# Optimization experiments

Measured on AMD Instinct MI355X. Metric: run time of the kernel, lower is better.

Reference implementation:

```python
import jax, jax.numpy as jnp
import numpy as np

H = 1024   # hidden size
E = 8      # num experts
B, S = 4, 2048


def setup_inputs() -> dict:
    key = jax.random.key(0)
    k1, k2, k3, k4 = jax.random.split(key, 4)
    x = jax.random.normal(k1, (B, S, H), dtype=jnp.float32)
    wg = jax.random.normal(k2, (H, E), dtype=jnp.float32) * 0.02      # gate weight
    W = jax.random.normal(k3, (E, H, H), dtype=jnp.float32) * 0.02    # expert Linear weights (out, in) per expert
    b = jax.random.normal(k4, (E, H), dtype=jnp.float32) * 0.02       # expert Linear biases
    return {"x": x, "wg": wg, "W": W, "b": b}


def reference(x, wg, W, b):
    Bb, Ss, Hh = x.shape
    Ee = wg.shape[1]
    T = Bb * Ss
    C = T // Ee  # capacity (capacity_factor = 1.0, top-1)

    xt = x.reshape(T, Hh)
    logits = xt @ wg                                   # [T, E]
    probs = jax.nn.softmax(logits, axis=-1)            # [T, E]
    idx = jnp.argmax(probs, axis=-1)                   # [T] top-1 expert
    mask = jax.nn.one_hot(idx, Ee, dtype=xt.dtype)     # [T, E]

    # position of each token within its expert's queue (0-based)
    locations = jnp.cumsum(mask, axis=0) - mask        # [T, E]
    # drop tokens over capacity
    mask = mask * (locations < C).astype(xt.dtype)
    gate = jnp.sum(probs * mask, axis=-1)              # [T] gate prob (0 if dropped)
    loc_s = jnp.sum(locations * mask, axis=-1).astype(jnp.int32)  # [T]
    loc_oh = jax.nn.one_hot(loc_s, C, dtype=xt.dtype)  # [T, C]

    dispatch = mask[:, :, None] * loc_oh[:, None, :]   # [T, E, C]
    combine = gate[:, None, None] * dispatch           # [T, E, C]

    # dispatch tokens -> per-expert buffers [E, C, H]
    exp_in = jnp.einsum('tec,th->ech', dispatch, xt)
    # per-expert Linear: y = x @ W_e^T + b_e
    exp_out = jnp.einsum('ech,efh->ecf', exp_in, W) + b[:, None, :]
    # combine back to tokens, scaled by gate prob
    out = jnp.einsum('tec,ecf->tf', combine, exp_out)  # [T, H]
    return out.reshape(Bb, Ss, Hh)
```

## Files before the change

### kernel.cpp

```cpp
#include <hip/hip_runtime.h>

#define H 1024
#define E 8
#define T 8192
#define CAP 1024

typedef __bf16 bf16x8 __attribute__((ext_vector_type(8)));
typedef float  f32x4  __attribute__((ext_vector_type(4)));
typedef unsigned short u16;

__device__ __forceinline__ u16 f2bf(float f) {
    union { float f; unsigned u; } v; v.f = f;
    unsigned r = v.u + 0x7FFFu + ((v.u >> 16) & 1u);
    return (u16)(r >> 16);
}

typedef __attribute__((address_space(1))) const void* gas_t;
typedef __attribute__((address_space(3))) void* las_t;
__device__ __forceinline__ void gld16(const void* g, void* l) {
    __builtin_amdgcn_global_load_lds((gas_t)g, (las_t)l, 16, 0, 0);
}

__global__ __launch_bounds__(256) void wgt_kernel(
    const float* __restrict__ wg, float* __restrict__ wgT) {
    const int h = blockIdx.x * 256 + threadIdx.x;
    float4 lo = *(const float4*)(wg + h * E);
    float4 hi = *(const float4*)(wg + h * E + 4);
    wgT[0 * H + h] = lo.x; wgT[1 * H + h] = lo.y;
    wgT[2 * H + h] = lo.z; wgT[3 * H + h] = lo.w;
    wgT[4 * H + h] = hi.x; wgT[5 * H + h] = hi.y;
    wgT[6 * H + h] = hi.z; wgT[7 * H + h] = hi.w;
}

#define GATE_BLOCKS 512
#define CVT_BLOCKS  1536

__global__ __launch_bounds__(256) void gatecvt_kernel(
    const float* __restrict__ x, const float* __restrict__ wgT,
    const float* __restrict__ W,
    int* __restrict__ eid, float* __restrict__ gate,
    u16* __restrict__ xbf, u16* __restrict__ Wbf) {
    const int tid = threadIdx.x;

    if (blockIdx.x >= GATE_BLOCKS) {
        int i = (blockIdx.x - GATE_BLOCKS) * 256 + tid;
        const int n4 = E * H * H / 4;
        const int stride = CVT_BLOCKS * 256;
        for (; i < n4; i += stride) {
            float4 v = ((const float4*)W)[i];
            ushort4 o;
            o.x = f2bf(v.x); o.y = f2bf(v.y); o.z = f2bf(v.z); o.w = f2bf(v.w);
            ((ushort4*)Wbf)[i] = o;
        }
        return;
    }

    const int wv = tid >> 6, lane = tid & 63;
    const int tbase = blockIdx.x * 16 + wv * 4;
    const int h00 = lane * 4;

    float a[4][8];
    #pragma unroll
    for (int j = 0; j < 4; ++j)
        #pragma unroll
        for (int e = 0; e < 8; ++e) a[j][e] = 0.f;

    #pragma unroll
    for (int q = 0; q < 4; ++q) {
        const int h0 = q * 256 + h00;
        float4 xv[4];
        #pragma unroll
        for (int j = 0; j < 4; ++j)
            xv[j] = *(const float4*)(x + (size_t)(tbase + j) * H + h0);
        #pragma unroll
        for (int j = 0; j < 4; ++j) {
            ushort4 o;
            o.x = f2bf(xv[j].x); o.y = f2bf(xv[j].y);
            o.z = f2bf(xv[j].z); o.w = f2bf(xv[j].w);
            *(ushort4*)(xbf + (size_t)(tbase + j) * H + h0) = o;
        }
        #pragma unroll
        for (int e = 0; e < 8; ++e) {
            const float4 w4 = *(const float4*)(wgT + e * H + h0);
            #pragma unroll
            for (int j = 0; j < 4; ++j)
                a[j][e] += xv[j].x * w4.x + xv[j].y * w4.y
                         + xv[j].z * w4.z + xv[j].w * w4.w;
        }
    }

    const bool b0 = lane & 1, b1 = lane & 2, b2 = lane & 4;
    const int elane = ((lane & 1) << 2) | (lane & 2) | ((lane >> 2) & 1);

    #pragma unroll
    for (int j = 0; j < 4; ++j) {
        float* A = a[j];
        #pragma unroll
        for (int k = 0; k < 4; ++k) {
            float t = b0 ? A[k] : A[k + 4];
            t = __shfl_xor(t, 1);
            A[k] = (b0 ? A[k + 4] : A[k]) + t;
        }
        #pragma unroll
        for (int k = 0; k < 2; ++k) {
            float t = b1 ? A[k] : A[k + 2];
            t = __shfl_xor(t, 2);
            A[k] = (b1 ? A[k + 2] : A[k]) + t;
        }
        {
            float t = b2 ? A[0] : A[1];
            t = __shfl_xor(t, 4);
            A[0] = (b2 ? A[1] : A[0]) + t;
        }
        float v = A[0];
        v += __shfl_xor(v, 8); v += __shfl_xor(v, 16); v += __shfl_xor(v, 32);
        float m = v; int mi = elane;
        #pragma unroll
        for (int off = 1; off <= 4; off <<= 1) {
            float om = __shfl_xor(m, off);
            int   oi = __shfl_xor(mi, off);
            if (om > m || (om == m && oi < mi)) { m = om; mi = oi; }
        }
        float s = expf(v - m);
        s += __shfl_xor(s, 1); s += __shfl_xor(s, 2); s += __shfl_xor(s, 4);
        if (lane == 0) {
            eid[tbase + j]  = mi;
            gate[tbase + j] = 1.0f / s;
        }
    }
}

#define TPT 32
__global__ __launch_bounds__(256) void scan_kernel(
    const int* __restrict__ eid, float* __restrict__ gate,
    int* __restrict__ perm) {
    __shared__ int cnt[256][E];
    __shared__ int base[256][E];
    __shared__ int part[E][8];
    const int tid = threadIdx.x;

    for (int i = tid; i < E * CAP; i += 256) perm[i] = -1;

    const int t0 = tid * TPT;
    int c[E];
    #pragma unroll
    for (int e = 0; e < E; ++e) c[e] = 0;
    for (int i = 0; i < TPT; ++i) {
        const int ei = eid[t0 + i];
        #pragma unroll
        for (int e = 0; e < E; ++e) c[e] += (ei == e);
    }
    #pragma unroll
    for (int e = 0; e < E; ++e) cnt[tid][e] = c[e];
    __syncthreads();
    if (tid < 64) {
        const int e = tid >> 3, j = tid & 7;
        int s = 0;
        for (int i = j * 32; i < j * 32 + 32; ++i) s += cnt[i][e];
        part[e][j] = s;
    }
    __syncthreads();
    if (tid < E) {
        int run = 0;
        #pragma unroll
        for (int j = 0; j < 8; ++j) { int v = part[tid][j]; part[tid][j] = run; run += v; }
    }
    __syncthreads();
    if (tid < 64) {
        const int e = tid >> 3, j = tid & 7;
        int run = part[e][j];
        for (int i = j * 32; i < j * 32 + 32; ++i) { base[i][e] = run; run += cnt[i][e]; }
    }
    __syncthreads();
    #pragma unroll
    for (int e = 0; e < E; ++e) c[e] = base[tid][e];
    for (int i = 0; i < TPT; ++i) {
        const int t = t0 + i;
        const int ei = eid[t];
        int pos = 0;
        #pragma unroll
        for (int e = 0; e < E; ++e) if (ei == e) pos = c[e]++;
        if (pos < CAP) perm[ei * CAP + pos] = t;
        else gate[t] = 0.f;
    }
}

__global__ __launch_bounds__(512, 4) void moe_gemm_bf(
    const u16* __restrict__ xbf, const u16* __restrict__ Wbf,
    const float* __restrict__ bias, const int* __restrict__ perm,
    const float* __restrict__ gate, float* __restrict__ out) {
    __shared__ __align__(16) u16 As[2][128 * 64];
    __shared__ __align__(16) u16 Bs[2][128 * 64];
    __shared__ int   perm_s[128];
    __shared__ float gate_s[128];

    const int tid = threadIdx.x;
    const int idx = blockIdx.x;

    if (idx >= 512) {
        const int t = (idx - 512) * 128 + (tid >> 2);
        if (gate[t] == 0.f) {
            const int part = tid & 3;
            float4 z = make_float4(0.f, 0.f, 0.f, 0.f);
            float4* o = (float4*)(out + (size_t)t * H + part * 256);
            #pragma unroll
            for (int i = 0; i < 64; ++i) o[i] = z;
        }
        return;
    }

    const int fb = idx >> 6;
    const int mb = (idx >> 3) & 7;
    const int e  = idx & 7;

    if (tid < 128) {
        const int t = perm[e * CAP + mb * 128 + tid];
        perm_s[tid] = t;
        gate_s[tid] = (t >= 0) ? gate[t] : 0.f;
    }
    __syncthreads();

    const int lane = tid & 63;
    const int wv = tid >> 6;
    const int wm = wv >> 2;
    const int wn = wv & 3;
    const int l16 = lane & 15, quad = lane >> 4;

    const int rl  = lane >> 3;
    const int cch = lane & 7;
    const int gch = cch ^ rl;
    const u16* ga[2]; const u16* gb[2];
    u16* la[2][2]; u16* lb[2][2];
    #pragma unroll
    for (int q = 0; q < 2; ++q) {
        const int r = wv * 16 + q * 8 + rl;
        const int tA = perm_s[r];
        const int tok = tA >= 0 ? tA : 0;
        ga[q] = xbf + (size_t)tok * H + gch * 8;
        gb[q] = Wbf + (size_t)e * H * H + (size_t)(fb * 128 + r) * H + gch * 8;
        #pragma unroll
        for (int bs = 0; bs < 2; ++bs) {
            la[bs][q] = &As[bs][(wv * 16 + q * 8) * 64 + lane * 8];
            lb[bs][q] = &Bs[bs][(wv * 16 + q * 8) * 64 + lane * 8];
        }
    }

    f32x4 acc[4][2] = {};
    const int NKT = H / 64;

    #pragma unroll
    for (int q = 0; q < 2; ++q) { gld16(ga[q], la[0][q]); gld16(gb[q], lb[0][q]); }

    for (int kt = 0; kt < NKT; ++kt) {
        const int bsel = kt & 1;
        __syncthreads();
        if (kt + 1 < NKT) {
            const int koff = (kt + 1) * 64;
            #pragma unroll
            for (int q = 0; q < 2; ++q) {
                gld16(ga[q] + koff, la[1 - bsel][q]);
                gld16(gb[q] + koff, lb[1 - bsel][q]);
            }
        }
        #pragma unroll
        for (int s = 0; s < 2; ++s) {
            bf16x8 af[4], bfr[2];
            const int cc = (s * 4 + quad) ^ (l16 & 7);
            #pragma unroll
            for (int i = 0; i < 4; ++i)
                af[i] = *(const bf16x8*)&As[bsel][(wm * 64 + i * 16 + l16) * 64 + cc * 8];
            #pragma unroll
            for (int i = 0; i < 2; ++i)
                bfr[i] = *(const bf16x8*)&Bs[bsel][(wn * 32 + i * 16 + l16) * 64 + cc * 8];
            #pragma unroll
            for (int mi = 0; mi < 4; ++mi)
                #pragma unroll
                for (int ni = 0; ni < 2; ++ni)
                    acc[mi][ni] = __builtin_amdgcn_mfma_f32_16x16x32_bf16(
                        af[mi], bfr[ni], acc[mi][ni], 0, 0, 0);
        }
    }

    float bv[2];
    #pragma unroll
    for (int ni = 0; ni < 2; ++ni)
        bv[ni] = bias[e * H + fb * 128 + wn * 32 + ni * 16 + l16];

    #pragma unroll
    for (int mi = 0; mi < 4; ++mi) {
        #pragma unroll
        for (int r = 0; r < 4; ++r) {
            const int rowl = wm * 64 + mi * 16 + quad * 4 + r;
            const int t = perm_s[rowl];
            if (t < 0) continue;
            const float g = gate_s[rowl];
            float* orow = out + (size_t)t * H + fb * 128 + wn * 32;
            #pragma unroll
            for (int ni = 0; ni < 2; ++ni)
                orow[ni * 16 + l16] = g * (acc[mi][ni][r] + bv[ni]);
        }
    }
}

extern "C" void kernel_launch(void* const* d_in, const int* in_sizes, int n_in,
                              void* d_out, int out_size, void* d_ws, size_t ws_size,
                              hipStream_t stream) {
    const float* x    = (const float*)d_in[0];
    const float* wg   = (const float*)d_in[1];
    const float* W    = (const float*)d_in[2];
    const float* bias = (const float*)d_in[3];
    float* out = (float*)d_out;

    int*   eid  = (int*)d_ws;
    float* gate = (float*)((char*)d_ws + (size_t)T * 4);
    int*   perm = (int*)((char*)d_ws + (size_t)T * 8);
    float* wgT  = (float*)((char*)d_ws + (size_t)T * 12);
    u16*   xbf  = (u16*)((char*)d_ws + (size_t)T * 12 + (size_t)E * H * 4);
    u16*   Wbf  = xbf + (size_t)T * H;

    wgt_kernel<<<H / 256, 256, 0, stream>>>(wg, wgT);
    gatecvt_kernel<<<GATE_BLOCKS + CVT_BLOCKS, 256, 0, stream>>>(
        x, wgT, W, eid, gate, xbf, Wbf);
    scan_kernel<<<1, 256, 0, stream>>>(eid, gate, perm);
    moe_gemm_bf<<<512 + 64, 512, 0, stream>>>(xbf, Wbf, bias, perm, gate, out);
}
```

Baseline: 156.2 us.

## Fuse fp32-to-bf16 weight conversion into the expert GEMM B-tile load

```diff
diff --git a/kernel.cpp b/kernel.cpp
--- a/kernel.cpp
+++ b/kernel.cpp
@@ -13,6 +13,11 @@
     union { float f; unsigned u; } v; v.f = f;
     unsigned r = v.u + 0x7FFFu + ((v.u >> 16) & 1u);
     return (u16)(r >> 16);
+}
+
+__device__ __forceinline__ unsigned pk2(float a, float b) {
+    union { float f; unsigned u; } x, y; x.f = a; y.f = b;
+    return ((x.u + 0x8000u) >> 16) | ((y.u + 0x8000u) & 0xFFFF0000u);
 }
 
 typedef __attribute__((address_space(1))) const void* gas_t;
@@ -32,29 +37,10 @@
     wgT[6 * H + h] = hi.z; wgT[7 * H + h] = hi.w;
 }
 
-#define GATE_BLOCKS 512
-#define CVT_BLOCKS  1536
-
-__global__ __launch_bounds__(256) void gatecvt_kernel(
+__global__ __launch_bounds__(256) void gate_kernel(
     const float* __restrict__ x, const float* __restrict__ wgT,
-    const float* __restrict__ W,
-    int* __restrict__ eid, float* __restrict__ gate,
-    u16* __restrict__ xbf, u16* __restrict__ Wbf) {
+    int* __restrict__ eid, float* __restrict__ gate, u16* __restrict__ xbf) {
     const int tid = threadIdx.x;
-
-    if (blockIdx.x >= GATE_BLOCKS) {
-        int i = (blockIdx.x - GATE_BLOCKS) * 256 + tid;
-        const int n4 = E * H * H / 4;
-        const int stride = CVT_BLOCKS * 256;
-        for (; i < n4; i += stride) {
-            float4 v = ((const float4*)W)[i];
-            ushort4 o;
-            o.x = f2bf(v.x); o.y = f2bf(v.y); o.z = f2bf(v.z); o.w = f2bf(v.w);
-            ((ushort4*)Wbf)[i] = o;
-        }
-        return;
-    }
-
     const int wv = tid >> 6, lane = tid & 63;
     const int tbase = blockIdx.x * 16 + wv * 4;
     const int h00 = lane * 4;
@@ -186,11 +172,11 @@
 }
 
 __global__ __launch_bounds__(512, 4) void moe_gemm_bf(
-    const u16* __restrict__ xbf, const u16* __restrict__ Wbf,
+    const u16* __restrict__ xbf, const float* __restrict__ W,
     const float* __restrict__ bias, const int* __restrict__ perm,
     const float* __restrict__ gate, float* __restrict__ out) {
     __shared__ __align__(16) u16 As[2][128 * 64];
-    __shared__ __align__(16) u16 Bs[2][128 * 64];
+    __shared__ __align__(16) u16 Bs[128 * 64];
     __shared__ int   perm_s[128];
     __shared__ float gate_s[128];
 
@@ -229,37 +215,51 @@
     const int rl  = lane >> 3;
     const int cch = lane & 7;
     const int gch = cch ^ rl;
-    const u16* ga[2]; const u16* gb[2];
-    u16* la[2][2]; u16* lb[2][2];
+    const u16*  ga[2];
+    const float* gbF[2];
+    u16* la[2][2];
+    u16* lb[2];
     #pragma unroll
     for (int q = 0; q < 2; ++q) {
         const int r = wv * 16 + q * 8 + rl;
         const int tA = perm_s[r];
         const int tok = tA >= 0 ? tA : 0;
-        ga[q] = xbf + (size_t)tok * H + gch * 8;
-        gb[q] = Wbf + (size_t)e * H * H + (size_t)(fb * 128 + r) * H + gch * 8;
-        #pragma unroll
-        for (int bs = 0; bs < 2; ++bs) {
-            la[bs][q] = &As[bs][(wv * 16 + q * 8) * 64 + lane * 8];
-            lb[bs][q] = &Bs[bs][(wv * 16 + q * 8) * 64 + lane * 8];
-        }
+        ga[q]  = xbf + (size_t)tok * H + gch * 8;
+        gbF[q] = W + (size_t)e * H * H + (size_t)(fb * 128 + r) * H + gch * 8;
+        la[0][q] = &As[0][(wv * 16 + q * 8) * 64 + lane * 8];
+        la[1][q] = &As[1][(wv * 16 + q * 8) * 64 + lane * 8];
+        lb[q]    = &Bs[(wv * 16 + q * 8) * 64 + lane * 8];
     }
 
     f32x4 acc[4][2] = {};
     const int NKT = H / 64;
-
-    #pragma unroll
-    for (int q = 0; q < 2; ++q) { gld16(ga[q], la[0][q]); gld16(gb[q], lb[0][q]); }
+    float4 bv[2][2];
+
+    #pragma unroll
+    for (int q = 0; q < 2; ++q) {
+        gld16(ga[q], la[0][q]);
+        bv[q][0] = *(const float4*)(gbF[q]);
+        bv[q][1] = *(const float4*)(gbF[q] + 4);
+    }
+    #pragma unroll
+    for (int q = 0; q < 2; ++q) {
+        uint4 p;
+        p.x = pk2(bv[q][0].x, bv[q][0].y);
+        p.y = pk2(bv[q][0].z, bv[q][0].w);
+        p.z = pk2(bv[q][1].x, bv[q][1].y);
+        p.w = pk2(bv[q][1].z, bv[q][1].w);
+        *(uint4*)lb[q] = p;
+    }
+    __syncthreads();
 
     for (int kt = 0; kt < NKT; ++kt) {
-        const int bsel = kt & 1;
-        __syncthreads();
+        const int c = kt & 1;
         if (kt + 1 < NKT) {
-            const int koff = (kt + 1) * 64;
             #pragma unroll
             for (int q = 0; q < 2; ++q) {
-                gld16(ga[q] + koff, la[1 - bsel][q]);
-                gld16(gb[q] + koff, lb[1 - bsel][q]);
+                gld16(ga[q] + (kt + 1) * 64, la[1 - c][q]);
+                bv[q][0] = *(const float4*)(gbF[q] + (kt + 1) * 64);
+                bv[q][1] = *(const float4*)(gbF[q] + (kt + 1) * 64 + 4);
             }
         }
         #pragma unroll
@@ -268,10 +268,10 @@
             const int cc = (s * 4 + quad) ^ (l16 & 7);
             #pragma unroll
             for (int i = 0; i < 4; ++i)
-                af[i] = *(const bf16x8*)&As[bsel][(wm * 64 + i * 16 + l16) * 64 + cc * 8];
+                af[i] = *(const bf16x8*)&As[c][(wm * 64 + i * 16 + l16) * 64 + cc * 8];
             #pragma unroll
             for (int i = 0; i < 2; ++i)
-                bfr[i] = *(const bf16x8*)&Bs[bsel][(wn * 32 + i * 16 + l16) * 64 + cc * 8];
+                bfr[i] = *(const bf16x8*)&Bs[(wn * 32 + i * 16 + l16) * 64 + cc * 8];
             #pragma unroll
             for (int mi = 0; mi < 4; ++mi)
                 #pragma unroll
@@ -279,12 +279,25 @@
                     acc[mi][ni] = __builtin_amdgcn_mfma_f32_16x16x32_bf16(
                         af[mi], bfr[ni], acc[mi][ni], 0, 0, 0);
         }
-    }
-
-    float bv[2];
+        __syncthreads();
+        if (kt + 1 < NKT) {
+            #pragma unroll
+            for (int q = 0; q < 2; ++q) {
+                uint4 p;
+                p.x = pk2(bv[q][0].x, bv[q][0].y);
+                p.y = pk2(bv[q][0].z, bv[q][0].w);
+                p.z = pk2(bv[q][1].x, bv[q][1].y);
+                p.w = pk2(bv[q][1].z, bv[q][1].w);
+                *(uint4*)lb[q] = p;
+            }
+            __syncthreads();
+        }
+    }
+
+    float bvv[2];
     #pragma unroll
     for (int ni = 0; ni < 2; ++ni)
-        bv[ni] = bias[e * H + fb * 128 + wn * 32 + ni * 16 + l16];
+        bvv[ni] = bias[e * H + fb * 128 + wn * 32 + ni * 16 + l16];
 
     #pragma unroll
     for (int mi = 0; mi < 4; ++mi) {
@@ -297,7 +310,7 @@
             float* orow = out + (size_t)t * H + fb * 128 + wn * 32;
             #pragma unroll
             for (int ni = 0; ni < 2; ++ni)
-                orow[ni * 16 + l16] = g * (acc[mi][ni][r] + bv[ni]);
+                orow[ni * 16 + l16] = g * (acc[mi][ni][r] + bvv[ni]);
         }
     }
 }
@@ -316,11 +329,9 @@
     int*   perm = (int*)((char*)d_ws + (size_t)T * 8);
     float* wgT  = (float*)((char*)d_ws + (size_t)T * 12);
     u16*   xbf  = (u16*)((char*)d_ws + (size_t)T * 12 + (size_t)E * H * 4);
-    u16*   Wbf  = xbf + (size_t)T * H;
 
     wgt_kernel<<<H / 256, 256, 0, stream>>>(wg, wgT);
-    gatecvt_kernel<<<GATE_BLOCKS + CVT_BLOCKS, 256, 0, stream>>>(
-        x, wgT, W, eid, gate, xbf, Wbf);
+    gate_kernel<<<512, 256, 0, stream>>>(x, wgT, eid, gate, xbf);
     scan_kernel<<<1, 256, 0, stream>>>(eid, gate, perm);
-    moe_gemm_bf<<<512 + 64, 512, 0, stream>>>(xbf, Wbf, bias, perm, gate, out);
-}
+    moe_gemm_bf<<<512 + 64, 512, 0, stream>>>(xbf, W, bias, perm, gate, out);
+}
```

Measured after the change: 169.2 us. 8.3% more time.
